# Performance work log

Hardware: AMD Instinct MI355X
Metric: run time of the kernel (lower is better)

Reference implementation:

```python
import math
from itertools import combinations
import jax, jax.numpy as jnp
import numpy as np

SEQ_LEN = 8
D_IN = 2048
D_OUT = 1152
TSS = 3          # temporal_set_size
WAY = 5
SHOT = 5
N_SUPPORT = WAY * SHOT
N_Q = 100
PE_SCALE = 0.1
LN_EPS = 1e-5

TUPLES = np.array(list(combinations(range(SEQ_LEN), TSS)), dtype=np.int32)  # [56, 3]
T_LEN = TUPLES.shape[0]  # 56


def _positional_encoding(seq_len, d):
    pos = np.arange(seq_len, dtype=np.float32)[:, None]
    div = np.exp(np.arange(0, d, 2, dtype=np.float32) * -(math.log(10000.0) / d))
    pe = np.zeros((seq_len, d), dtype=np.float32)
    pe[:, 0::2] = np.sin(pos * div) * PE_SCALE
    pe[:, 1::2] = np.cos(pos * div) * PE_SCALE
    return jnp.asarray(pe)


def _layernorm(x, g, b):
    mu = jnp.mean(x, axis=-1, keepdims=True)
    var = jnp.mean((x - mu) ** 2, axis=-1, keepdims=True)
    return (x - mu) * jax.lax.rsqrt(var + LN_EPS) * g + b


def setup_inputs() -> dict:
    key = jax.random.key(0)
    ks = jax.random.split(key, 6)
    support_set = jax.random.normal(ks[0], (N_SUPPORT, SEQ_LEN, D_IN), dtype=jnp.float32)
    queries = jax.random.normal(ks[1], (N_Q, SEQ_LEN, D_IN), dtype=jnp.float32)
    # sorted episode layout: class c occupies rows [c*SHOT, (c+1)*SHOT)
    support_labels = jnp.repeat(jnp.arange(WAY, dtype=jnp.int64), SHOT)
    d_flat = TSS * D_IN  # 6144
    k_w = jax.random.normal(ks[2], (d_flat, D_OUT), dtype=jnp.float32) * 0.02
    k_b = jnp.zeros((D_OUT,), dtype=jnp.float32)
    v_w = jax.random.normal(ks[3], (d_flat, D_OUT), dtype=jnp.float32) * 0.02
    v_b = jnp.zeros((D_OUT,), dtype=jnp.float32)
    ln_g = jnp.ones((D_OUT,), dtype=jnp.float32)
    ln_b = jnp.zeros((D_OUT,), dtype=jnp.float32)
    return {"support_set": support_set, "queries": queries,
            "support_labels": support_labels,
            "k_w": k_w, "k_b": k_b, "v_w": v_w, "v_b": v_b,
            "ln_g": ln_g, "ln_b": ln_b}


def reference(support_set, queries, support_labels, k_w, k_b, v_w, v_b, ln_g, ln_b):
    pe = _positional_encoding(SEQ_LEN, D_IN)  # dropout is identity in eval mode
    s = support_set + pe
    q = queries + pe

    def tuplify(x):  # [N, S, D] -> [N, T_LEN, TSS*D]
        return x[:, TUPLES, :].reshape(x.shape[0], T_LEN, TSS * D_IN)

    s_t = tuplify(s)
    q_t = tuplify(q)

    sk = _layernorm(s_t @ k_w + k_b, ln_g, ln_b)  # [25, 56, 1152]
    qk = _layernorm(q_t @ k_w + k_b, ln_g, ln_b)  # [100, 56, 1152]
    sv = s_t @ v_w + v_b                           # [25, 56, 1152]
    qv = q_t @ v_w + v_b                           # [100, 56, 1152]

    scale = 1.0 / math.sqrt(D_OUT)
    dists = []
    align = None
    for c in range(WAY):  # fixed small class loop; class rows are a static slice
        class_k = sk[c * SHOT:(c + 1) * SHOT]  # [SHOT, 56, 1152]
        class_v = sv[c * SHOT:(c + 1) * SHOT]
        # scores: [Q, T, K, T] == torch permute(0,2,1,3) of [Q, K, T, T]
        scores = jnp.einsum('qtd,ksd->qtks', qk, class_k) * scale
        flat = scores.reshape(N_Q, T_LEN, SHOT * T_LEN)
        sm = jax.nn.softmax(flat, axis=-1)
        sm = sm.reshape(N_Q, T_LEN, SHOT, T_LEN).transpose(0, 2, 1, 3)  # [Q, K, T, T]
        align = sm.sum(axis=1)  # [Q, T, T]
        proto = jnp.einsum('qkts,ksd->qtd', sm, class_v)  # [Q, 56, 1152]
        diff = qv - proto
        dists.append(-jnp.sum(diff * diff, axis=(-2, -1)) / T_LEN)  # [Q]
    logits = jnp.stack(dists, axis=1)  # [Q, WAY]
    return logits, align
```

## Files before the change

kernel.cpp:

```cpp
#include <hip/hip_runtime.h>
#include <hip/hip_bf16.h>
#include <math.h>

#define SEQ_LEN 8
#define D_IN 2048
#define D_OUT 1152
#define WAY 5
#define SHOT 5
#define N_SUPPORT 25
#define N_Q 100
#define N_SEQ 125
#define N_ROWS 1000
#define T_LEN 56
#define KS_LEN 280
#define KS_PAD 288
#define NCOLS 6912
#define MQT 5600
#define DPC 9

typedef __attribute__((ext_vector_type(4))) float f32x4;
typedef __attribute__((ext_vector_type(8))) short bf16x8;

__constant__ int TUP[T_LEN][3] = {
  {0,1,2},{0,1,3},{0,1,4},{0,1,5},{0,1,6},{0,1,7},{0,2,3},{0,2,4},{0,2,5},{0,2,6},
  {0,2,7},{0,3,4},{0,3,5},{0,3,6},{0,3,7},{0,4,5},{0,4,6},{0,4,7},{0,5,6},{0,5,7},
  {0,6,7},{1,2,3},{1,2,4},{1,2,5},{1,2,6},{1,2,7},{1,3,4},{1,3,5},{1,3,6},{1,3,7},
  {1,4,5},{1,4,6},{1,4,7},{1,5,6},{1,5,7},{1,6,7},{2,3,4},{2,3,5},{2,3,6},{2,3,7},
  {2,4,5},{2,4,6},{2,4,7},{2,5,6},{2,5,7},{2,6,7},{3,4,5},{3,4,6},{3,4,7},{3,5,6},
  {3,5,7},{3,6,7},{4,5,6},{4,5,7},{4,6,7},{5,6,7}
};

__device__ __forceinline__ ushort f2bf(float f) {
  union { float f; unsigned u; } v; v.f = f;
  unsigned r = v.u + 0x7FFFu + ((v.u >> 16) & 1u);
  return (ushort)(r >> 16);
}
__device__ __forceinline__ float bf2f(ushort u) {
  union { unsigned u; float f; } v; v.u = ((unsigned)u) << 16;
  return v.f;
}
__device__ __forceinline__ void gload16(const void* g, const void* l) {
  __builtin_amdgcn_global_load_lds(
      (const __attribute__((address_space(1))) unsigned int*)g,
      (__attribute__((address_space(3))) unsigned int*)l, 16, 0, 0);
}
template<int N> __device__ __forceinline__ void vmw() {
  asm volatile("s_waitcnt vmcnt(%0)" :: "n"(N) : "memory");
}
__device__ __forceinline__ void vmw_rt(int n) {
  switch (n) {
    case 0: vmw<0>(); break;
    case 3: vmw<3>(); break;
    case 4: vmw<4>(); break;
    case 6: vmw<6>(); break;
    case 8: vmw<8>(); break;
    default: vmw<0>(); break;
  }
}

__global__ __launch_bounds__(256) void pe_add(const float* __restrict__ sup,
                                              const float* __restrict__ que,
                                              ushort* __restrict__ X) {
  int idx = blockIdx.x * 256 + threadIdx.x;
  if (idx >= N_ROWS * D_IN) return;
  int d = idx & (D_IN - 1);
  int r = idx >> 11;
  int i = r & 7;
  int h2 = d & ~1;
  float freq = expf((float)h2 * (-9.210340371976184f / (float)D_IN));
  float ang = (float)i * freq;
  float pe = ((d & 1) ? cosf(ang) : sinf(ang)) * 0.1f;
  float src = (r < N_SUPPORT * SEQ_LEN) ? sup[idx] : que[idx - N_SUPPORT * SEQ_LEN * D_IN];
  X[idx] = f2bf(src + pe);
}

__global__ __launch_bounds__(256) void wtrans(const float* __restrict__ kw,
                                              const float* __restrict__ vw,
                                              ushort* __restrict__ WT) {
  __shared__ float tile[64][65];
  int bx = blockIdx.x;
  int by = blockIdx.y;
  int b = bx / 18;
  int n0 = (bx % 18) * 64;
  int k0 = by * 64;
  const float* src = ((b & 1) ? vw : kw) + (size_t)(b >> 1) * D_IN * D_OUT;
  int tid = threadIdx.x;
#pragma unroll
  for (int it = 0; it < 4; ++it) {
    int lin4 = it * 256 + tid;
    int kk = lin4 >> 4;
    int n4 = (lin4 & 15) * 4;
    float4 v = *(const float4*)(src + (size_t)(k0 + kk) * D_OUT + n0 + n4);
    tile[kk][n4 + 0] = v.x; tile[kk][n4 + 1] = v.y;
    tile[kk][n4 + 2] = v.z; tile[kk][n4 + 3] = v.w;
  }
  __syncthreads();
#pragma unroll
  for (int it = 0; it < 4; ++it) {
    int lin = it * 1024 + tid * 4;
    int nn = lin >> 6, kk = lin & 63;
    ushort4 o;
    o.x = f2bf(tile[kk + 0][nn]); o.y = f2bf(tile[kk + 1][nn]);
    o.z = f2bf(tile[kk + 2][nn]); o.w = f2bf(tile[kk + 3][nn]);
    *(ushort4*)&WT[((size_t)(b * D_OUT + n0 + nn)) * D_IN + k0 + kk] = o;
  }
}

template<int EPI, int NT, int DEPTH, int SWZ>
__global__ __launch_bounds__(256) void gemm_bt(
    const ushort* __restrict__ A, const ushort* __restrict__ BT,
    float* __restrict__ C,
    int M, int N, int K, int lda, int ldb, int ldc, float alpha,
    long batchA, long batchB, long batchC) {
  constexpr int JF = NT / 32;
  constexpr int NCH = 8 + NT / 16;
  __shared__ ushort As[DEPTH][128][32];
  __shared__ ushort Bs[DEPTH][NT][32];

  int bx, by, bz;
  if constexpr (SWZ == 1) {
    int L = blockIdx.x, xcd = L & 7, s = L >> 3;
    by = (s >> 3) * 8 + xcd;
    if (by >= 108) return;
    bx = s & 7; bz = 0;
  } else if constexpr (SWZ == 2) {
    int L = blockIdx.x, xcd = L & 7, s = L >> 3;
    bx = (s % 6) * 8 + xcd;
    if (bx >= 44) return;
    int g = s / 6; by = g % 3; bz = g / 3;
  } else { bx = blockIdx.x; by = blockIdx.y; bz = blockIdx.z; }

  A  += (size_t)bz * batchA;
  BT += (size_t)bz * batchB;
  C  += (size_t)bz * batchC;

  int tid = threadIdx.x;
  int wid = tid >> 6, lane = tid & 63;
  int l16 = lane & 15, lk = lane >> 4;
  int wr = wid >> 1, wc = wid & 1;
  int row0 = bx * 128, col0 = by * NT;
  int lrow = lane >> 2;
  int lcol = ((lane & 3) ^ ((lane >> 3) & 3)) * 8;
  int rslot = (lk ^ ((l16 >> 1) & 3)) * 8;

  auto stage = [&](int buf, int t) {
    int k0 = t * 32;
    for (int c = wid; c < NCH; c += 4) {
      if (c < 8) {
        int grow = row0 + c * 16 + lrow;
        grow = grow < M ? grow : M - 1;
        gload16(A + (size_t)grow * lda + k0 + lcol, &As[buf][c * 16][0]);
      } else {
        int gcol = col0 + (c - 8) * 16 + lrow;
        gcol = gcol < N ? gcol : N - 1;
        gload16(BT + (size_t)gcol * ldb + k0 + lcol, &Bs[buf][(c - 8) * 16][0]);
      }
    }
  };

  int perw = NCH / 4 + ((wid < (NCH & 3)) ? 1 : 0);
  f32x4 acc[4][JF] = {};
  int nk = K / 32;
#pragma unroll
  for (int i = 0; i < DEPTH - 1; ++i)
    if (i < nk) stage(i, i);
  for (int t = 0; t < nk; ++t) {
    int cur = t % DEPTH;
    int ts = t + DEPTH - 1;
    if (ts < nk) stage(ts % DEPTH, ts);
    int rem = nk - 1 - t; if (rem > DEPTH - 1) rem = DEPTH - 1;
    vmw_rt(rem * perw);
    __builtin_amdgcn_s_barrier();
    __builtin_amdgcn_sched_barrier(0);
    bf16x8 af[4], bv[JF];
#pragma unroll
    for (int m = 0; m < 4; ++m)
      af[m] = *(const bf16x8*)&As[cur][wr * 64 + m * 16 + l16][rslot];
#pragma unroll
    for (int j = 0; j < JF; ++j)
      bv[j] = *(const bf16x8*)&Bs[cur][wc * (NT / 2) + j * 16 + l16][rslot];
#pragma unroll
    for (int m = 0; m < 4; ++m)
#pragma unroll
      for (int j = 0; j < JF; ++j)
        acc[m][j] = __builtin_amdgcn_mfma_f32_16x16x32_bf16(af[m], bv[j], acc[m][j], 0, 0, 0);
    __builtin_amdgcn_sched_barrier(0);
    __builtin_amdgcn_s_barrier();
  }

#pragma unroll
  for (int m = 0; m < 4; ++m)
#pragma unroll
    for (int j = 0; j < JF; ++j) {
      int col = col0 + wc * (NT / 2) + j * 16 + l16;
#pragma unroll
      for (int r = 0; r < 4; ++r) {
        int row = row0 + wr * 64 + m * 16 + lk * 4 + r;
        if (row < M && col < N)
          C[(size_t)row * ldc + col] = (EPI == 1) ? acc[m][j][r] * alpha : acc[m][j][r];
      }
    }
}

__global__ __launch_bounds__(256) void pv_dist(const ushort* __restrict__ SM,
                                               const ushort* __restrict__ SVT,
                                               const ushort* __restrict__ QV,
                                               float* __restrict__ DP) {
  __shared__ ushort Bs[128][296];
  int L = blockIdx.x, xcd = L & 7, s = L >> 3;
  int bx = (s % 6) * 8 + xcd;
  if (bx >= 44) return;
  int g = s / 6; int by = g % 9, bz = g / 9;
  int tid = threadIdx.x, wid = tid >> 6, lane = tid & 63;
  int l16 = lane & 15, lk = lane >> 4;
  int row0 = bx * 128, col0 = by * 128, c = bz;
  const ushort* sm = SM + (size_t)c * MQT * KS_PAD;
  const ushort* bt = SVT + ((size_t)c * D_OUT + col0) * KS_PAD;
  {
    int r = tid >> 1, h = tid & 1;
    const ushort* srcr = bt + (size_t)r * KS_PAD + h * 144;
#pragma unroll
    for (int i = 0; i < 18; ++i) {
      uint4 v = *(const uint4*)(srcr + i * 8);
      *(uint4*)&Bs[r][h * 144 + i * 8] = v;
    }
  }
  __syncthreads();

  int ra0 = row0 + wid * 32 + l16;      if (ra0 > MQT - 1) ra0 = MQT - 1;
  int ra1 = row0 + wid * 32 + 16 + l16; if (ra1 > MQT - 1) ra1 = MQT - 1;
  const ushort* a0 = sm + (size_t)ra0 * KS_PAD + lk * 8;
  const ushort* a1 = sm + (size_t)ra1 * KS_PAD + lk * 8;

  f32x4 acc[2][8] = {};
#pragma unroll
  for (int ks = 0; ks < 9; ++ks) {
    bf16x8 af0 = *(const bf16x8*)(a0 + ks * 32);
    bf16x8 af1 = *(const bf16x8*)(a1 + ks * 32);
    bf16x8 bv[8];
#pragma unroll
    for (int j = 0; j < 8; ++j)
      bv[j] = *(const bf16x8*)&Bs[j * 16 + l16][ks * 32 + lk * 8];
#pragma unroll
    for (int j = 0; j < 8; ++j) {
      acc[0][j] = __builtin_amdgcn_mfma_f32_16x16x32_bf16(af0, bv[j], acc[0][j], 0, 0, 0);
      acc[1][j] = __builtin_amdgcn_mfma_f32_16x16x32_bf16(af1, bv[j], acc[1][j], 0, 0, 0);
    }
  }

  float sq[2][4] = {};
#pragma unroll
  for (int m = 0; m < 2; ++m)
#pragma unroll
    for (int r = 0; r < 4; ++r) {
      int row = row0 + wid * 32 + m * 16 + lk * 4 + r;
      int rowc = row < MQT ? row : MQT - 1;
      const ushort* qvr = QV + (size_t)rowc * D_OUT + col0;
#pragma unroll
      for (int j = 0; j < 8; ++j) {
        float qvv = bf2f(qvr[j * 16 + l16]);
        float d = qvv - acc[m][j][r];
        sq[m][r] += d * d;
      }
    }
#pragma unroll
  for (int m = 0; m < 2; ++m)
#pragma unroll
    for (int r = 0; r < 4; ++r) {
      sq[m][r] += __shfl_xor(sq[m][r], 1);
      sq[m][r] += __shfl_xor(sq[m][r], 2);
      sq[m][r] += __shfl_xor(sq[m][r], 4);
      sq[m][r] += __shfl_xor(sq[m][r], 8);
    }
  if (l16 == 0) {
    float* dp = DP + (size_t)c * MQT * DPC;
#pragma unroll
    for (int m = 0; m < 2; ++m)
#pragma unroll
      for (int r = 0; r < 4; ++r) {
        int row = row0 + wid * 32 + m * 16 + lk * 4 + r;
        if (row < MQT) dp[(size_t)row * DPC + by] = sq[m][r];
      }
  }
}

__global__ __launch_bounds__(256) void combine_ln(const float* __restrict__ G,
                                                  const float* __restrict__ kb,
                                                  const float* __restrict__ vb,
                                                  const float* __restrict__ lng,
                                                  const float* __restrict__ lnb,
                                                  ushort* __restrict__ skbf,
                                                  ushort* __restrict__ qkbf,
                                                  ushort* __restrict__ sv,
                                                  ushort* __restrict__ qvbf) {
  int L = blockIdx.x, xcd = L & 7, h = L >> 3;
  int n = (h / 14) * 8 + xcd;
  if (n >= N_SEQ) return;
  int t = (h % 14) * 4 + (threadIdx.x >> 6);
  int lane = threadIdx.x & 63;
  const float* g0 = G + (size_t)(n * 8 + TUP[t][0]) * NCOLS;
  const float* g1 = G + (size_t)(n * 8 + TUP[t][1]) * NCOLS + 2 * D_OUT;
  const float* g2 = G + (size_t)(n * 8 + TUP[t][2]) * NCOLS + 4 * D_OUT;
  bool isq = (n >= N_SUPPORT);
  int c = n / SHOT, s = n % SHOT;
  ushort* vout = isq ? qvbf + ((size_t)(n - N_SUPPORT) * T_LEN + t) * D_OUT
                     : sv + ((size_t)c * KS_PAD + s * T_LEN + t) * D_OUT;
  ushort* kout = isq ? qkbf + ((size_t)(n - N_SUPPORT) * T_LEN + t) * D_OUT
                     : skbf + ((size_t)c * KS_PAD + s * T_LEN + t) * D_OUT;
  float kvx[9], kvy[9], s1 = 0.f, s2 = 0.f;
#pragma unroll
  for (int i = 0; i < 9; ++i) {
    int d = i * 128 + lane * 2;
    float2 a = *(const float2*)(g0 + d);
    float2 b = *(const float2*)(g0 + D_OUT + d);
    float2 c1 = *(const float2*)(g1 + d);
    float2 c2 = *(const float2*)(g1 + D_OUT + d);
    float2 e1 = *(const float2*)(g2 + d);
    float2 e2 = *(const float2*)(g2 + D_OUT + d);
    float2 kb2 = *(const float2*)(kb + d);
    float2 vb2 = *(const float2*)(vb + d);
    float kx = a.x + c1.x + e1.x + kb2.x;
    float ky = a.y + c1.y + e1.y + kb2.y;
    float vx = b.x + c2.x + e2.x + vb2.x;
    float vy = b.y + c2.y + e2.y + vb2.y;
    kvx[i] = kx; kvy[i] = ky;
    ushort2 vv; vv.x = f2bf(vx); vv.y = f2bf(vy);
    *(ushort2*)(vout + d) = vv;
    s1 += kx + ky;
    s2 += kx * kx + ky * ky;
  }
#pragma unroll
  for (int m = 32; m > 0; m >>= 1) {
    s1 += __shfl_xor(s1, m);
    s2 += __shfl_xor(s2, m);
  }
  float mu = s1 * (1.0f / D_OUT);
  float var = s2 * (1.0f / D_OUT) - mu * mu;
  float rs = rsqrtf(var + 1e-5f);
#pragma unroll
  for (int i = 0; i < 9; ++i) {
    int d = i * 128 + lane * 2;
    float2 g2v = *(const float2*)(lng + d);
    float2 b2v = *(const float2*)(lnb + d);
    ushort2 o;
    o.x = f2bf((kvx[i] - mu) * rs * g2v.x + b2v.x);
    o.y = f2bf((kvy[i] - mu) * rs * g2v.y + b2v.y);
    *(ushort2*)(kout + d) = o;
  }
}

__global__ __launch_bounds__(256) void svtrans(const ushort* __restrict__ sv,
                                               ushort* __restrict__ svT) {
  __shared__ ushort tile[32][65];
  int c = blockIdx.z;
  int d0 = blockIdx.x * 64;
  int k0 = blockIdx.y * 32;
  const ushort* src = sv + (size_t)c * KS_PAD * D_OUT;
  ushort* dst = svT + (size_t)c * D_OUT * KS_PAD;
  int tid = threadIdx.x;
#pragma unroll
  for (int it = 0; it < 8; ++it) {
    int lin = it * 256 + tid;
    int ks = k0 + (lin >> 6), d = d0 + (lin & 63);
    tile[lin >> 6][lin & 63] = (ks < KS_LEN) ? src[(size_t)ks * D_OUT + d] : (ushort)0;
  }
  __syncthreads();
#pragma unroll
  for (int it = 0; it < 8; ++it) {
    int lin = it * 256 + tid;
    int d = lin >> 5, ks = lin & 31;
    dst[(size_t)(d0 + d) * KS_PAD + k0 + ks] = tile[ks][d];
  }
}

__global__ __launch_bounds__(256) void softmax_align(const float* __restrict__ S,
                                                     ushort* __restrict__ sm,
                                                     float* __restrict__ align_out) {
  __shared__ float pl[4][KS_LEN];
  int wid = threadIdx.x >> 6, lane = threadIdx.x & 63;
  int row = blockIdx.x * 4 + wid;
  const float* src = S + (size_t)row * KS_PAD;
  float v[5];
  float mx = -1e30f;
#pragma unroll
  for (int j = 0; j < 5; ++j) {
    int ks = lane + j * 64;
    v[j] = (ks < KS_LEN) ? src[ks] : -1e30f;
    mx = fmaxf(mx, v[j]);
  }
#pragma unroll
  for (int m = 32; m > 0; m >>= 1) mx = fmaxf(mx, __shfl_xor(mx, m));
  float sum = 0.f;
  float p[5];
#pragma unroll
  for (int j = 0; j < 5; ++j) {
    int ks = lane + j * 64;
    p[j] = (ks < KS_LEN) ? expf(v[j] - mx) : 0.f;
    sum += p[j];
  }
#pragma unroll
  for (int m = 32; m > 0; m >>= 1) sum += __shfl_xor(sum, m);
  float inv = 1.0f / sum;
  ushort* dst = sm + (size_t)row * KS_PAD;
#pragma unroll
  for (int j = 0; j < 5; ++j) {
    int ks = lane + j * 64;
    if (ks < KS_PAD) dst[ks] = f2bf((ks < KS_LEN) ? p[j] * inv : 0.f);
  }
  int c = row / MQT;
  if (c == WAY - 1) {
#pragma unroll
    for (int j = 0; j < 5; ++j) {
      int ks = lane + j * 64;
      if (ks < KS_LEN) pl[wid][ks] = p[j] * inv;
    }
    __syncthreads();
    if (lane < T_LEN) {
      float a = 0.f;
#pragma unroll
      for (int k = 0; k < SHOT; ++k) a += pl[wid][k * T_LEN + lane];
      int qt = row - (WAY - 1) * MQT;
      align_out[(size_t)(qt / T_LEN) * (T_LEN * T_LEN) + (qt % T_LEN) * T_LEN + lane] = a;
    }
  }
}

__global__ __launch_bounds__(256) void logits_k(const float* __restrict__ DP,
                                                float* __restrict__ out) {
  __shared__ float red[256];
  int q = blockIdx.x / WAY, c = blockIdx.x % WAY;
  const float* base = DP + ((size_t)c * MQT + q * T_LEN) * DPC;
  int tid = threadIdx.x;
  float s = 0.f;
  for (int i = tid; i < T_LEN * DPC; i += 256) s += base[i];
  red[tid] = s;
  __syncthreads();
  for (int sft = 128; sft > 0; sft >>= 1) {
    if (tid < sft) red[tid] += red[tid + sft];
    __syncthreads();
  }
  if (tid == 0) out[blockIdx.x] = -red[0] * (1.0f / T_LEN);
}

extern "C" void kernel_launch(void* const* d_in, const int* in_sizes, int n_in,
                              void* d_out, int out_size, void* d_ws, size_t ws_size,
                              hipStream_t stream) {
  const float* sup  = (const float*)d_in[0];
  const float* que  = (const float*)d_in[1];
  const float* k_w  = (const float*)d_in[3];
  const float* k_b  = (const float*)d_in[4];
  const float* v_w  = (const float*)d_in[5];
  const float* v_b  = (const float*)d_in[6];
  const float* ln_g = (const float*)d_in[7];
  const float* ln_b = (const float*)d_in[8];
  float* out = (float*)d_out;

  char* w = (char*)d_ws;
  ushort* Xbf  = (ushort*)(w + 0);
  ushort* WT   = (ushort*)(w + 4096000);
  float*  G    = (float*)(w + 32407552);
  ushort* sv   = (ushort*)(w + 0);
  float*  S    = (float*)(w + 0);
  ushort* smbf = (ushort*)(w + 32407552);
  float*  DP   = (float*)(w + 0);
  ushort* qkbf = (ushort*)(w + 60055552);
  ushort* skbf = (ushort*)(w + 72957952);
  ushort* svT  = (ushort*)(w + 76275712);
  ushort* qvbf = (ushort*)(w + 79593472);

  const float scale = 0.02946278254943948f;

  pe_add<<<dim3(8000), 256, 0, stream>>>(sup, que, Xbf);
  wtrans<<<dim3(108, 32), 256, 0, stream>>>(k_w, v_w, WT);
  gemm_bt<0, 64, 3, 1><<<dim3(896), 256, 0, stream>>>(
      Xbf, WT, G,
      N_ROWS, NCOLS, D_IN, D_IN, D_IN, NCOLS, 1.0f, 0, 0, 0);
  combine_ln<<<dim3(1792), 256, 0, stream>>>(
      G, k_b, v_b, ln_g, ln_b, skbf, qkbf, sv, qvbf);
  svtrans<<<dim3(18, 9, WAY), 256, 0, stream>>>(sv, svT);
  gemm_bt<1, 96, 2, 2><<<dim3(720), 256, 0, stream>>>(
      qkbf, skbf, S,
      MQT, KS_PAD, D_OUT, D_OUT, D_OUT, KS_PAD, scale,
      0, (long)KS_PAD * D_OUT, (long)MQT * KS_PAD);
  softmax_align<<<dim3(7000), 256, 0, stream>>>(S, smbf, out + N_Q * WAY);
  pv_dist<<<dim3(2160), 256, 0, stream>>>(smbf, svT, qvbf, DP);
  logits_k<<<dim3(N_Q * WAY), 256, 0, stream>>>(DP, out);
}
```

Measured before the change: 195.5 us.

## Add dedicated projection GEMM with wider tiles and vectorized PE add

```diff
diff --git a/kernel.cpp b/kernel.cpp
--- a/kernel.cpp
+++ b/kernel.cpp
@@ -58,20 +58,33 @@
   }
 }
 
-__global__ __launch_bounds__(256) void pe_add(const float* __restrict__ sup,
-                                              const float* __restrict__ que,
-                                              ushort* __restrict__ X) {
+__global__ __launch_bounds__(256) void pe_table(float* __restrict__ PE) {
   int idx = blockIdx.x * 256 + threadIdx.x;
-  if (idx >= N_ROWS * D_IN) return;
-  int d = idx & (D_IN - 1);
-  int r = idx >> 11;
-  int i = r & 7;
+  if (idx >= SEQ_LEN * D_IN) return;
+  int d = idx & (D_IN - 1), i = idx >> 11;
   int h2 = d & ~1;
   float freq = expf((float)h2 * (-9.210340371976184f / (float)D_IN));
   float ang = (float)i * freq;
-  float pe = ((d & 1) ? cosf(ang) : sinf(ang)) * 0.1f;
-  float src = (r < N_SUPPORT * SEQ_LEN) ? sup[idx] : que[idx - N_SUPPORT * SEQ_LEN * D_IN];
-  X[idx] = f2bf(src + pe);
+  PE[idx] = ((d & 1) ? cosf(ang) : sinf(ang)) * 0.1f;
+}
+
+__global__ __launch_bounds__(256) void pe_add4(const float* __restrict__ sup,
+                                               const float* __restrict__ que,
+                                               const float* __restrict__ PE,
+                                               ushort* __restrict__ X) {
+  int idx = blockIdx.x * 256 + threadIdx.x;
+  if (idx >= N_ROWS * D_IN / 4) return;
+  int d4 = idx & (D_IN / 4 - 1);
+  int r = idx >> 9;
+  int i = r & 7;
+  float4 p = *(const float4*)(PE + (size_t)i * D_IN + d4 * 4);
+  float4 v = (r < N_SUPPORT * SEQ_LEN)
+                 ? *(const float4*)(sup + (size_t)idx * 4)
+                 : *(const float4*)(que + (size_t)idx * 4 - (size_t)N_SUPPORT * SEQ_LEN * D_IN);
+  ushort4 o;
+  o.x = f2bf(v.x + p.x); o.y = f2bf(v.y + p.y);
+  o.z = f2bf(v.z + p.z); o.w = f2bf(v.w + p.w);
+  *(ushort4*)(X + (size_t)idx * 4) = o;
 }
 
 __global__ __launch_bounds__(256) void wtrans(const float* __restrict__ kw,
@@ -106,6 +119,84 @@
   }
 }
 
+__global__ __launch_bounds__(256) void proj3(const ushort* __restrict__ A,
+                                             const ushort* __restrict__ BT,
+                                             float* __restrict__ G) {
+  constexpr int DEPTH = 3;
+  __shared__ ushort As[DEPTH][128][32];
+  __shared__ ushort Bs[DEPTH][96][32];
+  int L = blockIdx.x, xcd = L & 7, s = L >> 3;
+  int pair = (s % 9) * 8 + xcd;
+  int brow = s / 9;
+  int ct = pair >> 1, kv = pair & 1;
+  int col0 = ct * 32;
+  int row0 = brow * 128;
+
+  int tid = threadIdx.x;
+  int wid = tid >> 6, lane = tid & 63;
+  int l16 = lane & 15, lk = lane >> 4;
+  int wr = wid >> 1, wc = wid & 1;
+  int lrow = lane >> 2;
+  int lcol = ((lane & 3) ^ ((lane >> 3) & 3)) * 8;
+  int rslot = (lk ^ ((l16 >> 1) & 3)) * 8;
+
+  auto stage = [&](int buf, int t) {
+    int k0 = t * 32;
+    for (int c = wid; c < 14; c += 4) {
+      if (c < 8) {
+        int grow = row0 + c * 16 + lrow;
+        grow = grow < N_ROWS ? grow : N_ROWS - 1;
+        gload16(A + (size_t)grow * D_IN + k0 + lcol, &As[buf][c * 16][0]);
+      } else {
+        int cb = c - 8;
+        int slot = cb >> 1, half = cb & 1;
+        int grow = (2 * slot + kv) * D_OUT + col0 + half * 16 + lrow;
+        gload16(BT + (size_t)grow * D_IN + k0 + lcol, &Bs[buf][cb * 16][0]);
+      }
+    }
+  };
+
+  int perw = 3 + (wid < 2 ? 1 : 0);
+  f32x4 acc[4][3] = {};
+  stage(0, 0);
+  stage(1, 1);
+  for (int t = 0; t < 64; ++t) {
+    int cur = t % DEPTH;
+    int ts = t + 2;
+    if (ts < 64) stage(ts % DEPTH, ts);
+    int rem = 63 - t; if (rem > 2) rem = 2;
+    vmw_rt(rem * perw);
+    __builtin_amdgcn_s_barrier();
+    __builtin_amdgcn_sched_barrier(0);
+    bf16x8 af[4], bv[3];
+#pragma unroll
+    for (int m = 0; m < 4; ++m)
+      af[m] = *(const bf16x8*)&As[cur][wr * 64 + m * 16 + l16][rslot];
+#pragma unroll
+    for (int s3 = 0; s3 < 3; ++s3)
+      bv[s3] = *(const bf16x8*)&Bs[cur][s3 * 32 + wc * 16 + l16][rslot];
+#pragma unroll
+    for (int m = 0; m < 4; ++m)
+#pragma unroll
+      for (int s3 = 0; s3 < 3; ++s3)
+        acc[m][s3] = __builtin_amdgcn_mfma_f32_16x16x32_bf16(af[m], bv[s3], acc[m][s3], 0, 0, 0);
+    __builtin_amdgcn_sched_barrier(0);
+    __builtin_amdgcn_s_barrier();
+  }
+
+#pragma unroll
+  for (int s3 = 0; s3 < 3; ++s3) {
+    int col = (2 * s3 + kv) * D_OUT + col0 + wc * 16 + l16;
+#pragma unroll
+    for (int m = 0; m < 4; ++m)
+#pragma unroll
+      for (int r = 0; r < 4; ++r) {
+        int row = row0 + wr * 64 + m * 16 + lk * 4 + r;
+        if (row < N_ROWS) G[(size_t)row * NCOLS + col] = acc[m][s3][r];
+      }
+  }
+}
+
 template<int EPI, int NT, int DEPTH, int SWZ>
 __global__ __launch_bounds__(256) void gemm_bt(
     const ushort* __restrict__ A, const ushort* __restrict__ BT,
@@ -118,12 +209,7 @@
   __shared__ ushort Bs[DEPTH][NT][32];
 
   int bx, by, bz;
-  if constexpr (SWZ == 1) {
-    int L = blockIdx.x, xcd = L & 7, s = L >> 3;
-    by = (s >> 3) * 8 + xcd;
-    if (by >= 108) return;
-    bx = s & 7; bz = 0;
-  } else if constexpr (SWZ == 2) {
+  if constexpr (SWZ == 2) {
     int L = blockIdx.x, xcd = L & 7, s = L >> 3;
     bx = (s % 6) * 8 + xcd;
     if (bx >= 44) return;
@@ -457,6 +543,7 @@
 
   char* w = (char*)d_ws;
   ushort* Xbf  = (ushort*)(w + 0);
+  float*  PEt  = (float*)(w + 4096000);
   ushort* WT   = (ushort*)(w + 4096000);
   float*  G    = (float*)(w + 32407552);
   ushort* sv   = (ushort*)(w + 0);
@@ -470,15 +557,14 @@
 
   const float scale = 0.02946278254943948f;
 
-  pe_add<<<dim3(8000), 256, 0, stream>>>(sup, que, Xbf);
+  pe_table<<<dim3(64), 256, 0, stream>>>(PEt);
+  pe_add4<<<dim3(2000), 256, 0, stream>>>(sup, que, PEt, Xbf);
   wtrans<<<dim3(108, 32), 256, 0, stream>>>(k_w, v_w, WT);
-  gemm_bt<0, 64, 3, 1><<<dim3(896), 256, 0, stream>>>(
-      Xbf, WT, G,
-      N_ROWS, NCOLS, D_IN, D_IN, D_IN, NCOLS, 1.0f, 0, 0, 0);
+  proj3<<<dim3(576), 256, 0, stream>>>(Xbf, WT, G);
   combine_ln<<<dim3(1792), 256, 0, stream>>>(
       G, k_b, v_b, ln_g, ln_b, skbf, qkbf, sv, qvbf);
   svtrans<<<dim3(18, 9, WAY), 256, 0, stream>>>(sv, svT);
-  gemm_bt<1, 96, 2, 2><<<dim3(720), 256, 0, stream>>>(
+  gemm_bt<1, 96, 3, 2><<<dim3(720), 256, 0, stream>>>(
       qkbf, skbf, S,
       MQT, KS_PAD, D_OUT, D_OUT, D_OUT, KS_PAD, scale,
       0, (long)KS_PAD * D_OUT, (long)MQT * KS_PAD);
```

Result: slower. 213.1 us (+9.0%).
